# Kernel tuning notes

Measured on AMD Instinct MI355X. Metric: run time of the kernel, lower is better.

## Reference

```python
import jax, jax.numpy as jnp
import numpy as np

EPS = 1e-5
N_GROUPS = 32
N_HEAD = 1


def group_norm(x, gamma, beta):
    B, C, H, W = x.shape
    xg = x.reshape(B, N_GROUPS, C // N_GROUPS, H, W)
    mean = xg.mean(axis=(2, 3, 4), keepdims=True)
    var = xg.var(axis=(2, 3, 4), keepdims=True)
    xg = (xg - mean) * jax.lax.rsqrt(var + EPS)
    x = xg.reshape(B, C, H, W)
    return x * gamma[None, :, None, None] + beta[None, :, None, None]


def setup_inputs() -> dict:
    key = jax.random.key(0)
    k1, k2, k3 = jax.random.split(key, 3)
    B, C, H, W = 32, 512, 32, 32
    x = jax.random.normal(k1, (B, C, H, W), dtype=jnp.float32)
    gamma = jnp.ones((C,), dtype=jnp.float32)
    beta = jnp.zeros((C,), dtype=jnp.float32)
    # fan_avg uniform init for 1x1 convs (bound = sqrt(3*scale/fan_avg))
    bound_qkv = np.sqrt(3.0 / ((C + 3 * C) / 2))
    w_qkv = jax.random.uniform(k2, (3 * C, C), dtype=jnp.float32,
                               minval=-bound_qkv, maxval=bound_qkv)
    b_qkv = jnp.zeros((3 * C,), dtype=jnp.float32)
    bound_out = np.sqrt(3.0 * 1e-10 / C)
    w_out = jax.random.uniform(k3, (C, C), dtype=jnp.float32,
                               minval=-bound_out, maxval=bound_out)
    b_out = jnp.zeros((C,), dtype=jnp.float32)
    return {"x": x, "gamma": gamma, "beta": beta,
            "w_qkv": w_qkv, "b_qkv": b_qkv, "w_out": w_out, "b_out": b_out}


def reference(x, gamma, beta, w_qkv, b_qkv, w_out, b_out):
    B, C, H, W = x.shape
    n_head = N_HEAD
    head_dim = C // n_head
    norm = group_norm(x, gamma, beta)
    # 1x1 conv == channel matmul: [B,3C,H,W]
    qkv = jnp.einsum('bchw,oc->bohw', norm, w_qkv) + b_qkv[None, :, None, None]
    qkv = qkv.reshape(B, n_head, 3 * head_dim, H, W)
    q, k, v = jnp.split(qkv, 3, axis=2)  # each [B,n,hd,H,W]
    scale = 1.0 / np.sqrt(head_dim)
    attn = jnp.einsum('bnchw,bncyx->bnhwyx', q, k) * scale
    attn = jax.nn.softmax(attn.reshape(B, n_head, H, W, H * W), axis=-1)
    attn = attn.reshape(B, n_head, H, W, H, W)
    out = jnp.einsum('bnhwyx,bncyx->bnchw', attn, v).reshape(B, C, H, W)
    out = jnp.einsum('bchw,oc->bohw', out, w_out) + b_out[None, :, None, None]
    return out + x
```

## Files before the change

kernel.cpp:

```cpp
#include <hip/hip_runtime.h>
#include <hip/hip_bf16.h>

#define B_    32
#define C_    512
#define S_    1024
#define G_    32
#define CPG_  16
#define EPS_  1e-5f
#define SCALE_ 0.044194173824159216f

typedef __attribute__((ext_vector_type(4))) float  floatx4;
typedef __attribute__((ext_vector_type(8))) __bf16 bf16x8;

__device__ __forceinline__ float bf2f(unsigned short u) {
    union { unsigned int i; float f; } v; v.i = ((unsigned int)u) << 16; return v.f;
}
__device__ __forceinline__ unsigned short f2bf(float f) {
    union { float f; unsigned int i; } v; v.f = f;
    unsigned int r = v.i + 0x7fffu + ((v.i >> 16) & 1u);
    return (unsigned short)(r >> 16);
}

__device__ __forceinline__ void gl16(const unsigned short* g, unsigned short* l) {
    __builtin_amdgcn_global_load_lds(
        (const __attribute__((address_space(1))) unsigned int*)g,
        (__attribute__((address_space(3))) unsigned int*)l, 16, 0, 0);
}

__global__ __launch_bounds__(256) void gnxnt(const float* __restrict__ x,
                                             const float* __restrict__ gamma,
                                             const float* __restrict__ beta,
                                             unsigned short* __restrict__ xnt,
                                             float* __restrict__ lbuf) {
    const int bid = blockIdx.x;
    const int b = bid >> 5, g = bid & 31;
    if (threadIdx.x < 8)
        ((float4*)lbuf)[bid * 8 + threadIdx.x] = make_float4(0.f, 0.f, 0.f, 0.f);

    __shared__ float tile[16 * 1025];
    __shared__ float a1[4], a2[4];
    const float* xb = x + (size_t)b * (C_ * S_) + (size_t)g * (CPG_ * S_);
    const int t = threadIdx.x;

    float s = 0.f, ss = 0.f;
    #pragma unroll
    for (int k = 0; k < 16; k++) {
        int idx = t + k * 256;
        float4 v = ((const float4*)xb)[idx];
        int c = idx >> 8, s4 = (idx & 255) * 4;
        float* dst = tile + c * 1025 + s4;
        dst[0] = v.x; dst[1] = v.y; dst[2] = v.z; dst[3] = v.w;
        s  += v.x + v.y + v.z + v.w;
        ss += v.x * v.x + v.y * v.y + v.z * v.z + v.w * v.w;
    }
    #pragma unroll
    for (int o = 32; o; o >>= 1) { s += __shfl_down(s, o); ss += __shfl_down(ss, o); }
    const int wid = t >> 6, lane = t & 63;
    if (lane == 0) { a1[wid] = s; a2[wid] = ss; }
    __syncthreads();
    float S  = a1[0] + a1[1] + a1[2] + a1[3];
    float SS = a2[0] + a2[1] + a2[2] + a2[3];
    float mean = S * (1.f / 16384.f);
    float var  = SS * (1.f / 16384.f) - mean * mean;
    float rstd = rsqrtf(var + EPS_);

    const int c0 = g * 16, cc = (t & 3) * 4;
    float av[4], bv[4];
    #pragma unroll
    for (int i = 0; i < 4; i++) {
        float a_ = rstd * gamma[c0 + cc + i];
        av[i] = a_; bv[i] = beta[c0 + cc + i] - mean * a_;
    }
    unsigned short* xo = xnt + (size_t)b * (S_ * C_) + c0 + cc;
    #pragma unroll
    for (int p = 0; p < 16; p++) {
        int srow = p * 64 + (t >> 2);
        const float* col = tile + srow;
        ushort4 o4;
        o4.x = f2bf(av[0] * col[(cc + 0) * 1025] + bv[0]);
        o4.y = f2bf(av[1] * col[(cc + 1) * 1025] + bv[1]);
        o4.z = f2bf(av[2] * col[(cc + 2) * 1025] + bv[2]);
        o4.w = f2bf(av[3] * col[(cc + 3) * 1025] + bv[3]);
        *(ushort4*)(xo + (size_t)srow * C_) = o4;
    }
}

__global__ __launch_bounds__(256) void tcast(const float* __restrict__ w,
                                             const float* __restrict__ w_out,
                                             unsigned short* __restrict__ WqT,
                                             unsigned short* __restrict__ WkT,
                                             unsigned short* __restrict__ WvT,
                                             unsigned short* __restrict__ Woutb) {
    const int z = blockIdx.z;
    const int m0 = blockIdx.y * 64, c0 = blockIdx.x * 64;
    const int t = threadIdx.x, tr = t >> 4, tc4 = (t & 15) * 4;
    if (z == 3) {
        #pragma unroll
        for (int i = 0; i < 4; i++) {
            int r = tr + i * 16;
            float4 v = *(const float4*)(w_out + (size_t)(m0 + r) * 512 + c0 + tc4);
            ushort4 o4;
            o4.x = f2bf(v.x); o4.y = f2bf(v.y); o4.z = f2bf(v.z); o4.w = f2bf(v.w);
            *(ushort4*)(Woutb + (size_t)(m0 + r) * 512 + c0 + tc4) = o4;
        }
        return;
    }
    const float* src = w + (size_t)z * 262144;
    unsigned short* dst = (z == 0) ? WqT : (z == 1) ? WkT : WvT;
    __shared__ float tile[64][65];
    #pragma unroll
    for (int i = 0; i < 4; i++) {
        int r = tr + i * 16;
        float4 v = *(const float4*)(src + (size_t)(m0 + r) * 512 + c0 + tc4);
        tile[r][tc4 + 0] = v.x; tile[r][tc4 + 1] = v.y;
        tile[r][tc4 + 2] = v.z; tile[r][tc4 + 3] = v.w;
    }
    __syncthreads();
    #pragma unroll
    for (int i = 0; i < 4; i++) {
        int sr = tr + i * 16;
        ushort4 o4;
        o4.x = f2bf(tile[tc4 + 0][sr]); o4.y = f2bf(tile[tc4 + 1][sr]);
        o4.z = f2bf(tile[tc4 + 2][sr]); o4.w = f2bf(tile[tc4 + 3][sr]);
        *(ushort4*)(dst + (size_t)(c0 + sr) * 512 + m0 + tc4) = o4;
    }
}

__global__ __launch_bounds__(256) void vecprep(const unsigned short* __restrict__ WkT,
                                               const float* __restrict__ w_out,
                                               const float* __restrict__ b_qkv,
                                               float* __restrict__ bzv) {
    const int o = blockIdx.x, t = threadIdx.x;
    float us = 0.f, bv = 0.f;
    #pragma unroll
    for (int mm = 0; mm < 2; mm++) {
        int m = t + mm * 256;
        us += b_qkv[m] * bf2f(WkT[(size_t)o * 512 + m]);
        bv += w_out[(size_t)o * 512 + m] * b_qkv[1024 + m];
    }
    #pragma unroll
    for (int sh = 32; sh; sh >>= 1) { us += __shfl_down(us, sh); bv += __shfl_down(bv, sh); }
    __shared__ float a[2][4];
    const int wid = t >> 6, lane = t & 63;
    if (lane == 0) { a[0][wid] = us; a[1][wid] = bv; }
    __syncthreads();
    if (t == 0) {
        bzv[o]       = (a[0][0] + a[0][1] + a[0][2] + a[0][3]) * SCALE_;
        bzv[512 + o] =  a[1][0] + a[1][1] + a[1][2] + a[1][3];
    }
}

template<bool SWAP>
__device__ __forceinline__ void mfma_loop(const unsigned short* __restrict__ Ag, int lda,
                                          const unsigned short* __restrict__ Bg, int ldb,
                                          int K, int m0, int n0,
                                          unsigned short* ldsA, unsigned short* ldsB,
                                          floatx4 (&acc)[4][4]) {
    const int t = threadIdx.x, lane = t & 63, wave = t >> 6;
    const int wr = (wave >> 1) * 64, wc = (wave & 1) * 64;
    const int lrow = lane & 15, lq = lane >> 4;
    const int srow = wave * 16 + (lane >> 2);
    const int scol = (lane & 3) * 8;
    const unsigned short* gA0 = Ag + (size_t)(m0 + srow) * lda + scol;
    const unsigned short* gA1 = gA0 + (size_t)64 * lda;
    const unsigned short* gB0 = Bg + (size_t)(n0 + srow) * ldb + scol;
    const unsigned short* gB1 = gB0 + (size_t)64 * ldb;
    unsigned short* lA = ldsA + wave * 512;
    unsigned short* lB = ldsB + wave * 512;
    for (int k0 = 0; k0 < K; k0 += 64) {
        gl16(gA0 + k0,      lA);
        gl16(gA1 + k0,      lA + 2048);
        gl16(gA0 + k0 + 32, lA + 4096);
        gl16(gA1 + k0 + 32, lA + 6144);
        gl16(gB0 + k0,      lB);
        gl16(gB1 + k0,      lB + 2048);
        gl16(gB0 + k0 + 32, lB + 4096);
        gl16(gB1 + k0 + 32, lB + 6144);
        __syncthreads();
        #pragma unroll
        for (int sub = 0; sub < 2; sub++) {
            bf16x8 af[4], bfr[4];
            #pragma unroll
            for (int i = 0; i < 4; i++) {
                af[i]  = *(const bf16x8*)(ldsA + sub * 4096 + (wr + i * 16 + lrow) * 32 + lq * 8);
                bfr[i] = *(const bf16x8*)(ldsB + sub * 4096 + (wc + i * 16 + lrow) * 32 + lq * 8);
            }
            #pragma unroll
            for (int i = 0; i < 4; i++)
                #pragma unroll
                for (int j = 0; j < 4; j++) {
                    if (SWAP)
                        acc[i][j] = __builtin_amdgcn_mfma_f32_16x16x32_bf16(bfr[j], af[i], acc[i][j], 0, 0, 0);
                    else
                        acc[i][j] = __builtin_amdgcn_mfma_f32_16x16x32_bf16(af[i], bfr[j], acc[i][j], 0, 0, 0);
                }
        }
        __syncthreads();
    }
}

__global__ __launch_bounds__(256) void prep_gemm(const unsigned short* __restrict__ WkT,
                                                 const unsigned short* __restrict__ WqT,
                                                 const unsigned short* __restrict__ Woutb,
                                                 const unsigned short* __restrict__ WvT,
                                                 unsigned short* __restrict__ Wzv) {
    __shared__ __align__(16) unsigned short ldsA[2 * 128 * 32];
    __shared__ __align__(16) unsigned short ldsB[2 * 128 * 32];
    const int z = blockIdx.z;
    const int m0 = blockIdx.y * 128, n0 = blockIdx.x * 128;
    const int t = threadIdx.x, lane = t & 63, wave = t >> 6;
    const int wr = (wave >> 1) * 64, wc = (wave & 1) * 64;
    const int lrow = lane & 15, lq = lane >> 4;
    floatx4 acc[4][4];
    #pragma unroll
    for (int i = 0; i < 4; i++)
        #pragma unroll
        for (int j = 0; j < 4; j++) acc[i][j] = (floatx4){0.f, 0.f, 0.f, 0.f};
    const unsigned short* Ag = z ? Woutb : WkT;
    const unsigned short* Bg = z ? WvT   : WqT;
    mfma_loop<true>(Ag, 512, Bg, 512, 512, m0, n0, ldsA, ldsB, acc);
    const float sc = z ? 1.f : SCALE_;
    #pragma unroll
    for (int i = 0; i < 4; i++)
        #pragma unroll
        for (int j = 0; j < 4; j++) {
            int row = z * 512 + m0 + wr + i * 16 + lrow;
            int col = n0 + wc + j * 16 + lq * 4;
            floatx4 v = acc[i][j];
            ushort4 o4;
            o4.x = f2bf(v[0] * sc); o4.y = f2bf(v[1] * sc);
            o4.z = f2bf(v[2] * sc); o4.w = f2bf(v[3] * sc);
            *(ushort4*)(Wzv + (size_t)row * 512 + col) = o4;
        }
}

template<bool SWAP>
__device__ __forceinline__ void mfma256_loop(const unsigned short* __restrict__ Ag, int lda,
                                             const unsigned short* __restrict__ Bg, int ldb,
                                             int nt, int m0, int n0,
                                             unsigned short* lds, floatx4 (&acc)[8][4]) {
    const int tid  = threadIdx.x;
    const int lane = tid & 63, wave = tid >> 6;
    const int wm = wave >> 2, wn = wave & 3;
    const int lrow = lane & 15, lq = lane >> 4;
    const int cs = lq ^ ((lrow >> 1) & 3);

    int aofs[8], bofs[4];
    #pragma unroll
    for (int i = 0; i < 8; i++) aofs[i] = (wm * 128 + i * 16 + lrow) * 32 + cs * 8;
    #pragma unroll
    for (int j = 0; j < 4; j++) bofs[j] = (wn * 64 + j * 16 + lrow) * 32 + cs * 8;

    const int sr  = tid >> 2;
    const int scs = (tid & 3) ^ ((tid >> 3) & 3);
    const unsigned short* gA = Ag + (size_t)(m0 + sr) * lda + scs * 8;
    const unsigned short* gB = Bg + (size_t)(n0 + sr) * ldb + scs * 8;
    const size_t a128 = (size_t)128 * lda, b128 = (size_t)128 * ldb;
    unsigned short* lwA = lds + wave * 512;
    unsigned short* lwB = lds + 32768 + wave * 512;

#define STAGE_A(t, kh) do { \
    unsigned short* lb_ = lwA + ((t) & 1) * 16384 + (kh) * 8192; \
    const unsigned short* gp_ = gA + (t) * 64 + (kh) * 32; \
    gl16(gp_, lb_); gl16(gp_ + a128, lb_ + 4096); } while (0)
#define STAGE_B(t, kh) do { \
    unsigned short* lb_ = lwB + ((t) & 1) * 16384 + (kh) * 8192; \
    const unsigned short* gp_ = gB + (t) * 64 + (kh) * 32; \
    gl16(gp_, lb_); gl16(gp_ + b128, lb_ + 4096); } while (0)

    STAGE_A(0, 0); STAGE_B(0, 0); STAGE_A(0, 1); STAGE_B(0, 1);
    STAGE_A(1, 0); STAGE_B(1, 0);
    asm volatile("s_waitcnt vmcnt(4)" ::: "memory");
    __builtin_amdgcn_s_barrier();

    bf16x8 af[4], bfr[4];
    for (int u = 0; u < nt; ++u) {
        const int p = u & 1;
        #pragma unroll
        for (int ph = 0; ph < 4; ++ph) {
            const int kh = ph >> 1, mh = ph & 1;
            const int slab = p * 16384 + kh * 8192;
            if (mh == 0) {
                #pragma unroll
                for (int j = 0; j < 4; j++)
                    bfr[j] = *(const bf16x8*)(lds + 32768 + slab + bofs[j]);
            }
            #pragma unroll
            for (int i = 0; i < 4; i++)
                af[i] = *(const bf16x8*)(lds + slab + aofs[mh * 4 + i]);
            if (ph == 0)      { if (u + 1 < nt) STAGE_A(u + 1, 1); }
            else if (ph == 1) { if (u + 1 < nt) STAGE_B(u + 1, 1); }
            else if (ph == 2) { if (u + 2 < nt) STAGE_A(u + 2, 0); }
            else              { if (u + 2 < nt) STAGE_B(u + 2, 0); }
            __builtin_amdgcn_s_barrier();
            asm volatile("s_waitcnt lgkmcnt(0)" ::: "memory");
            __builtin_amdgcn_sched_barrier(0);
            __builtin_amdgcn_s_setprio(1);
            #pragma unroll
            for (int i = 0; i < 4; i++)
                #pragma unroll
                for (int j = 0; j < 4; j++) {
                    if (SWAP)
                        acc[mh * 4 + i][j] = __builtin_amdgcn_mfma_f32_16x16x32_bf16(
                            bfr[j], af[i], acc[mh * 4 + i][j], 0, 0, 0);
                    else
                        acc[mh * 4 + i][j] = __builtin_amdgcn_mfma_f32_16x16x32_bf16(
                            af[i], bfr[j], acc[mh * 4 + i][j], 0, 0, 0);
                }
            __builtin_amdgcn_s_setprio(0);
            if (ph < 3) {
                __builtin_amdgcn_s_barrier();
            } else if (u < nt - 2) {
                asm volatile("s_waitcnt vmcnt(4)" ::: "memory");
                __builtin_amdgcn_s_barrier();
            } else if (u == nt - 2) {
                asm volatile("s_waitcnt vmcnt(0)" ::: "memory");
                __builtin_amdgcn_s_barrier();
            }
        }
    }
#undef STAGE_A
#undef STAGE_B
}

#define GEMM256_VARS                                                  \
    __shared__ __align__(16) unsigned short lds[65536];               \
    const int lane = threadIdx.x & 63, wave = threadIdx.x >> 6;       \
    const int wm = wave >> 2, wn = wave & 3;                          \
    const int lrow = lane & 15, lq = lane >> 4;                       \
    floatx4 acc[8][4];                                                \
    _Pragma("unroll") for (int i = 0; i < 8; i++)                     \
        _Pragma("unroll") for (int j = 0; j < 4; j++)                 \
            acc[i][j] = (floatx4){0.f, 0.f, 0.f, 0.f};

__global__ __launch_bounds__(512, 2) void zv_mfma(const unsigned short* __restrict__ Wzv,
                                                  const unsigned short* __restrict__ xnt,
                                                  const float* __restrict__ bzv,
                                                  unsigned short* __restrict__ Zb,
                                                  unsigned short* __restrict__ Vb) {
    const int f = blockIdx.x;
    const int xcd = f & 7, j = f >> 3;
    const int b = xcd + 8 * (j >> 4);
    const int tile = j & 15;
    const int m0 = (tile >> 2) * 256, n0 = (tile & 3) * 256;
    GEMM256_VARS
    const unsigned short* Bg = xnt + (size_t)b * (S_ * C_);
    if (m0 < 512) {
        mfma256_loop<false>(Wzv, C_, Bg, C_, 8, m0, n0, lds, acc);
        unsigned short* dst = Zb + (size_t)b * (S_ * C_);
        #pragma unroll
        for (int i = 0; i < 8; i++)
            #pragma unroll
            for (int j2 = 0; j2 < 4; j2++) {
                int oabs = m0 + wm * 128 + i * 16 + lq * 4;
                int s    = n0 + wn * 64 + j2 * 16 + lrow;
                float4 bi = *(const float4*)(bzv + oabs);
                floatx4 v = acc[i][j2];
                ushort4 o4;
                o4.x = f2bf(v[0] + bi.x); o4.y = f2bf(v[1] + bi.y);
                o4.z = f2bf(v[2] + bi.z); o4.w = f2bf(v[3] + bi.w);
                *(ushort4*)(dst + (size_t)s * C_ + oabs) = o4;
            }
    } else {
        mfma256_loop<true>(Wzv, C_, Bg, C_, 8, m0, n0, lds, acc);
        unsigned short* dst = Vb + (size_t)b * (C_ * S_);
        #pragma unroll
        for (int i = 0; i < 8; i++)
            #pragma unroll
            for (int j2 = 0; j2 < 4; j2++) {
                int row = m0 + wm * 128 + i * 16 + lrow;
                int c   = row - 512;
                int sb  = n0 + wn * 64 + j2 * 16 + lq * 4;
                float bi = bzv[row];
                floatx4 v = acc[i][j2];
                ushort4 o4;
                o4.x = f2bf(v[0] + bi); o4.y = f2bf(v[1] + bi);
                o4.z = f2bf(v[2] + bi); o4.w = f2bf(v[3] + bi);
                *(ushort4*)(dst + (size_t)c * S_ + sb) = o4;
            }
    }
}

__global__ __launch_bounds__(512, 2) void scores_exp(const unsigned short* __restrict__ Zb,
                                                     const unsigned short* __restrict__ xnt,
                                                     unsigned short* __restrict__ Pb,
                                                     float* __restrict__ l) {
    const int f = blockIdx.x;
    const int xcd = f & 7, j = f >> 3;
    const int b = xcd + 8 * (j >> 4);
    const int tile = j & 15;
    const int m0 = (tile >> 2) * 256, n0 = (tile & 3) * 256;
    GEMM256_VARS
    const unsigned short* Ag = Zb  + (size_t)b * (S_ * C_);
    const unsigned short* Bg = xnt + (size_t)b * (S_ * C_);
    mfma256_loop<true>(Ag, C_, Bg, C_, 8, m0, n0, lds, acc);
    unsigned short* pp = Pb + (size_t)b * (S_ * S_);
    float* lb = l + b * S_;
    float rsv[8];
    #pragma unroll
    for (int i = 0; i < 8; i++) {
        int q = m0 + wm * 128 + i * 16 + lrow;
        float rs = 0.f;
        #pragma unroll
        for (int j2 = 0; j2 < 4; j2++) {
            int kv = n0 + wn * 64 + j2 * 16 + lq * 4;
            floatx4 v = acc[i][j2];
            float e0 = __expf(v[0]), e1 = __expf(v[1]);
            float e2 = __expf(v[2]), e3 = __expf(v[3]);
            rs += (e0 + e1) + (e2 + e3);
            ushort4 o4;
            o4.x = f2bf(e0); o4.y = f2bf(e1); o4.z = f2bf(e2); o4.w = f2bf(e3);
            *(ushort4*)(pp + (size_t)q * S_ + kv) = o4;
        }
        rs += __shfl_xor(rs, 16);
        rs += __shfl_xor(rs, 32);
        rsv[i] = rs;
    }
    __syncthreads();
    float* sred = (float*)lds;
    if (lane < 16) {
        #pragma unroll
        for (int i = 0; i < 8; i++)
            sred[wn * 256 + wm * 128 + i * 16 + lrow] = rsv[i];
    }
    __syncthreads();
    if (threadIdx.x < 256) {
        int q = threadIdx.x;
        float sum = (sred[q] + sred[256 + q]) + (sred[512 + q] + sred[768 + q]);
        atomicAdd(lb + m0 + q, sum);
    }
}

__global__ __launch_bounds__(512, 2) void pv_out(const unsigned short* __restrict__ Vb,
                                                 const unsigned short* __restrict__ Pb,
                                                 const float* __restrict__ l,
                                                 const float* __restrict__ bout,
                                                 const float* __restrict__ x,
                                                 float* __restrict__ out) {
    const int f = blockIdx.x;
    const int xcd = f & 7, j = f >> 3;
    const int b = xcd + 8 * (j >> 3);
    const int tile = j & 7;
    const int m0 = (tile & 1) * 256, n0 = (tile >> 1) * 256;
    GEMM256_VARS
    const unsigned short* Ag = Vb + (size_t)b * (C_ * S_);
    const unsigned short* Bg = Pb + (size_t)b * (S_ * S_);
    mfma256_loop<true>(Ag, S_, Bg, S_, 16, m0, n0, lds, acc);
    const float* lb = l + b * S_;
    const float* xb = x + (size_t)b * (C_ * S_);
    float* ob = out + (size_t)b * (C_ * S_);
    #pragma unroll
    for (int i = 0; i < 8; i++) {
        int c = m0 + wm * 128 + i * 16 + lrow;
        float bb = bout[c];
        #pragma unroll
        for (int j2 = 0; j2 < 4; j2++) {
            int s = n0 + wn * 64 + j2 * 16 + lq * 4;
            float4 lv = *(const float4*)(lb + s);
            size_t idx = (size_t)c * S_ + s;
            float4 xv = *(const float4*)(xb + idx);
            floatx4 v = acc[i][j2];
            float4 r;
            r.x = v[0] * __frcp_rn(lv.x) + bb + xv.x;
            r.y = v[1] * __frcp_rn(lv.y) + bb + xv.y;
            r.z = v[2] * __frcp_rn(lv.z) + bb + xv.z;
            r.w = v[3] * __frcp_rn(lv.w) + bb + xv.w;
            *(float4*)(ob + idx) = r;
        }
    }
}

extern "C" void kernel_launch(void* const* d_in, const int* in_sizes, int n_in,
                              void* d_out, int out_size, void* d_ws, size_t ws_size,
                              hipStream_t stream) {
    const float* x      = (const float*)d_in[0];
    const float* gamma  = (const float*)d_in[1];
    const float* beta   = (const float*)d_in[2];
    const float* w_qkv  = (const float*)d_in[3];
    const float* b_qkv  = (const float*)d_in[4];
    const float* w_out  = (const float*)d_in[5];
    const float* b_out  = (const float*)d_in[6];
    float* out          = (float*)d_out;

    char* ws = (char*)d_ws;
    unsigned short* Zb    = (unsigned short*)(ws);
    unsigned short* Vb    = (unsigned short*)(ws + 33554432ULL);
    unsigned short* xnt   = (unsigned short*)(ws + 67108864ULL);
    unsigned short* Pb    = (unsigned short*)(ws + 100663296ULL);
    unsigned short* WqT   = (unsigned short*)(ws + 167772160ULL);
    unsigned short* WkT   = (unsigned short*)(ws + 167772160ULL + 524288ULL);
    unsigned short* WvT   = (unsigned short*)(ws + 167772160ULL + 1048576ULL);
    unsigned short* Woutb = (unsigned short*)(ws + 167772160ULL + 1572864ULL);
    unsigned short* Wzv   = (unsigned short*)(ws + 167772160ULL + 2097152ULL);
    float*          bzv   = (float*)(ws + 167772160ULL + 3145728ULL);
    float*          lbuf  = (float*)(ws + 167772160ULL + 3162112ULL);

    gnxnt    <<<B_ * G_, 256, 0, stream>>>(x, gamma, beta, xnt, lbuf);
    tcast    <<<dim3(8, 8, 4), 256, 0, stream>>>(w_qkv, w_out, WqT, WkT, WvT, Woutb);
    prep_gemm<<<dim3(4, 4, 2), 256, 0, stream>>>(WkT, WqT, Woutb, WvT, Wzv);
    vecprep  <<<512, 256, 0, stream>>>(WkT, w_out, b_qkv, bzv);
    zv_mfma  <<<512, 512, 0, stream>>>(Wzv, xnt, bzv, Zb, Vb);
    scores_exp<<<512, 512, 0, stream>>>(Zb, xnt, Pb, lbuf);
    pv_out   <<<256, 512, 0, stream>>>(Vb, Pb, lbuf, b_out, x, out);
}
```

Baseline: 305.0 us.

## Switch attention GEMM pipeline from bf16 to fp8 with scaling factors

Converts the normalized activations, fused weights, Z/V intermediates and the exponentiated score matrix from bf16 to fp8, and replaces the bf16 MFMA loop with an fp8 16x16x32 MFMA loop using 8-byte operand fragments and a byte-oriented LDS layout. Power-of-two scale factors keep the small-magnitude Z and V values in fp8 range and are undone in the softmax and output epilogues. This halves global and LDS traffic and doubles MFMA throughput per byte. The cost is much lower precision in the score and probability matrices, which may hurt accuracy.

```diff
diff --git a/kernel.cpp b/kernel.cpp
--- a/kernel.cpp
+++ b/kernel.cpp
@@ -8,9 +8,14 @@
 #define CPG_  16
 #define EPS_  1e-5f
 #define SCALE_ 0.044194173824159216f
+#define ZS_    1024.0f
+#define VS_    1048576.0f
+#define INVZS_ 0.0009765625f
+#define INVVS_ 9.5367431640625e-07f
 
 typedef __attribute__((ext_vector_type(4))) float  floatx4;
 typedef __attribute__((ext_vector_type(8))) __bf16 bf16x8;
+typedef long lng;
 
 __device__ __forceinline__ float bf2f(unsigned short u) {
     union { unsigned int i; float f; } v; v.i = ((unsigned int)u) << 16; return v.f;
@@ -20,8 +25,13 @@
     unsigned int r = v.i + 0x7fffu + ((v.i >> 16) & 1u);
     return (unsigned short)(r >> 16);
 }
-
-__device__ __forceinline__ void gl16(const unsigned short* g, unsigned short* l) {
+__device__ __forceinline__ unsigned int f2f8x4(float a, float b, float c, float d) {
+    unsigned int v = (unsigned int)__builtin_amdgcn_cvt_pk_fp8_f32(a, b, 0, false);
+    v = (unsigned int)__builtin_amdgcn_cvt_pk_fp8_f32(c, d, (int)v, true);
+    return v;
+}
+
+__device__ __forceinline__ void gl16(const void* g, void* l) {
     __builtin_amdgcn_global_load_lds(
         (const __attribute__((address_space(1))) unsigned int*)g,
         (__attribute__((address_space(3))) unsigned int*)l, 16, 0, 0);
@@ -30,7 +40,7 @@
 __global__ __launch_bounds__(256) void gnxnt(const float* __restrict__ x,
                                              const float* __restrict__ gamma,
                                              const float* __restrict__ beta,
-                                             unsigned short* __restrict__ xnt,
+                                             unsigned char* __restrict__ xnt,
                                              float* __restrict__ lbuf) {
     const int bid = blockIdx.x;
     const int b = bid >> 5, g = bid & 31;
@@ -71,17 +81,16 @@
         float a_ = rstd * gamma[c0 + cc + i];
         av[i] = a_; bv[i] = beta[c0 + cc + i] - mean * a_;
     }
-    unsigned short* xo = xnt + (size_t)b * (S_ * C_) + c0 + cc;
+    unsigned char* xo = xnt + (size_t)b * (S_ * C_) + c0 + cc;
     #pragma unroll
     for (int p = 0; p < 16; p++) {
         int srow = p * 64 + (t >> 2);
         const float* col = tile + srow;
-        ushort4 o4;
-        o4.x = f2bf(av[0] * col[(cc + 0) * 1025] + bv[0]);
-        o4.y = f2bf(av[1] * col[(cc + 1) * 1025] + bv[1]);
-        o4.z = f2bf(av[2] * col[(cc + 2) * 1025] + bv[2]);
-        o4.w = f2bf(av[3] * col[(cc + 3) * 1025] + bv[3]);
-        *(ushort4*)(xo + (size_t)srow * C_) = o4;
+        unsigned int o4 = f2f8x4(av[0] * col[(cc + 0) * 1025] + bv[0],
+                                 av[1] * col[(cc + 1) * 1025] + bv[1],
+                                 av[2] * col[(cc + 2) * 1025] + bv[2],
+                                 av[3] * col[(cc + 3) * 1025] + bv[3]);
+        *(unsigned int*)(xo + (size_t)srow * C_) = o4;
     }
 }
 
@@ -145,8 +154,8 @@
     if (lane == 0) { a[0][wid] = us; a[1][wid] = bv; }
     __syncthreads();
     if (t == 0) {
-        bzv[o]       = (a[0][0] + a[0][1] + a[0][2] + a[0][3]) * SCALE_;
-        bzv[512 + o] =  a[1][0] + a[1][1] + a[1][2] + a[1][3];
+        bzv[o]       = (a[0][0] + a[0][1] + a[0][2] + a[0][3]) * SCALE_ * ZS_;
+        bzv[512 + o] = (a[1][0] + a[1][1] + a[1][2] + a[1][3]) * VS_;
     }
 }
 
@@ -203,7 +212,7 @@
                                                  const unsigned short* __restrict__ WqT,
                                                  const unsigned short* __restrict__ Woutb,
                                                  const unsigned short* __restrict__ WvT,
-                                                 unsigned short* __restrict__ Wzv) {
+                                                 unsigned char* __restrict__ Wzv) {
     __shared__ __align__(16) unsigned short ldsA[2 * 128 * 32];
     __shared__ __align__(16) unsigned short ldsB[2 * 128 * 32];
     const int z = blockIdx.z;
@@ -219,7 +228,7 @@
     const unsigned short* Ag = z ? Woutb : WkT;
     const unsigned short* Bg = z ? WvT   : WqT;
     mfma_loop<true>(Ag, 512, Bg, 512, 512, m0, n0, ldsA, ldsB, acc);
-    const float sc = z ? 1.f : SCALE_;
+    const float sc = z ? VS_ : (SCALE_ * ZS_);
     #pragma unroll
     for (int i = 0; i < 4; i++)
         #pragma unroll
@@ -227,67 +236,73 @@
             int row = z * 512 + m0 + wr + i * 16 + lrow;
             int col = n0 + wc + j * 16 + lq * 4;
             floatx4 v = acc[i][j];
-            ushort4 o4;
-            o4.x = f2bf(v[0] * sc); o4.y = f2bf(v[1] * sc);
-            o4.z = f2bf(v[2] * sc); o4.w = f2bf(v[3] * sc);
-            *(ushort4*)(Wzv + (size_t)row * 512 + col) = o4;
+            unsigned int o4 = f2f8x4(v[0] * sc, v[1] * sc, v[2] * sc, v[3] * sc);
+            *(unsigned int*)(Wzv + (size_t)row * 512 + col) = o4;
         }
 }
 
 template<bool SWAP>
-__device__ __forceinline__ void mfma256_loop(const unsigned short* __restrict__ Ag, int lda,
-                                             const unsigned short* __restrict__ Bg, int ldb,
-                                             int nt, int m0, int n0,
-                                             unsigned short* lds, floatx4 (&acc)[8][4]) {
+__device__ __forceinline__ void mfma256f8_loop(const unsigned char* __restrict__ Ag, int lda,
+                                               const unsigned char* __restrict__ Bg, int ldb,
+                                               int nt, int m0, int n0,
+                                               unsigned char* lds, floatx4 (&acc)[8][4]) {
     const int tid  = threadIdx.x;
     const int lane = tid & 63, wave = tid >> 6;
     const int wm = wave >> 2, wn = wave & 3;
     const int lrow = lane & 15, lq = lane >> 4;
-    const int cs = lq ^ ((lrow >> 1) & 3);
-
-    int aofs[8], bofs[4];
-    #pragma unroll
-    for (int i = 0; i < 8; i++) aofs[i] = (wm * 128 + i * 16 + lrow) * 32 + cs * 8;
-    #pragma unroll
-    for (int j = 0; j < 4; j++) bofs[j] = (wn * 64 + j * 16 + lrow) * 32 + cs * 8;
+    const int swz  = (lrow >> 1) & 3;
+    const int hb   = (lq & 1) * 8;
+    const int slb  = lq >> 1;
+    const int s0 = ((slb    ) ^ swz) * 16 + hb;
+    const int s1 = ((slb + 2) ^ swz) * 16 + hb;
+
+    int aof[8], bof[4];
+    #pragma unroll
+    for (int i = 0; i < 8; i++) aof[i] = (wm * 128 + i * 16 + lrow) * 64;
+    #pragma unroll
+    for (int j = 0; j < 4; j++) bof[j] = 65536 + (wn * 64 + j * 16 + lrow) * 64;
 
     const int sr  = tid >> 2;
     const int scs = (tid & 3) ^ ((tid >> 3) & 3);
-    const unsigned short* gA = Ag + (size_t)(m0 + sr) * lda + scs * 8;
-    const unsigned short* gB = Bg + (size_t)(n0 + sr) * ldb + scs * 8;
+    const unsigned char* gA = Ag + (size_t)(m0 + sr) * lda + scs * 16;
+    const unsigned char* gB = Bg + (size_t)(n0 + sr) * ldb + scs * 16;
     const size_t a128 = (size_t)128 * lda, b128 = (size_t)128 * ldb;
-    unsigned short* lwA = lds + wave * 512;
-    unsigned short* lwB = lds + 32768 + wave * 512;
+    unsigned char* lwA = lds + wave * 1024;
+    unsigned char* lwB = lds + 65536 + wave * 1024;
 
 #define STAGE_A(t, kh) do { \
-    unsigned short* lb_ = lwA + ((t) & 1) * 16384 + (kh) * 8192; \
-    const unsigned short* gp_ = gA + (t) * 64 + (kh) * 32; \
-    gl16(gp_, lb_); gl16(gp_ + a128, lb_ + 4096); } while (0)
+    unsigned char* lb_ = lwA + ((t) & 1) * 32768 + (kh) * 16384; \
+    const unsigned char* gp_ = gA + (t) * 128 + (kh) * 64; \
+    gl16(gp_, lb_); gl16(gp_ + a128, lb_ + 8192); } while (0)
 #define STAGE_B(t, kh) do { \
-    unsigned short* lb_ = lwB + ((t) & 1) * 16384 + (kh) * 8192; \
-    const unsigned short* gp_ = gB + (t) * 64 + (kh) * 32; \
-    gl16(gp_, lb_); gl16(gp_ + b128, lb_ + 4096); } while (0)
+    unsigned char* lb_ = lwB + ((t) & 1) * 32768 + (kh) * 16384; \
+    const unsigned char* gp_ = gB + (t) * 128 + (kh) * 64; \
+    gl16(gp_, lb_); gl16(gp_ + b128, lb_ + 8192); } while (0)
 
     STAGE_A(0, 0); STAGE_B(0, 0); STAGE_A(0, 1); STAGE_B(0, 1);
     STAGE_A(1, 0); STAGE_B(1, 0);
     asm volatile("s_waitcnt vmcnt(4)" ::: "memory");
     __builtin_amdgcn_s_barrier();
 
-    bf16x8 af[4], bfr[4];
+    lng af0[4], af1[4], bf0[4], bf1[4];
     for (int u = 0; u < nt; ++u) {
         const int p = u & 1;
         #pragma unroll
         for (int ph = 0; ph < 4; ++ph) {
             const int kh = ph >> 1, mh = ph & 1;
-            const int slab = p * 16384 + kh * 8192;
+            const int slab = p * 32768 + kh * 16384;
             if (mh == 0) {
                 #pragma unroll
-                for (int j = 0; j < 4; j++)
-                    bfr[j] = *(const bf16x8*)(lds + 32768 + slab + bofs[j]);
+                for (int j = 0; j < 4; j++) {
+                    bf0[j] = *(const lng*)(lds + slab + bof[j] + s0);
+                    bf1[j] = *(const lng*)(lds + slab + bof[j] + s1);
+                }
             }
             #pragma unroll
-            for (int i = 0; i < 4; i++)
-                af[i] = *(const bf16x8*)(lds + slab + aofs[mh * 4 + i]);
+            for (int i = 0; i < 4; i++) {
+                af0[i] = *(const lng*)(lds + slab + aof[mh * 4 + i] + s0);
+                af1[i] = *(const lng*)(lds + slab + aof[mh * 4 + i] + s1);
+            }
             if (ph == 0)      { if (u + 1 < nt) STAGE_A(u + 1, 1); }
             else if (ph == 1) { if (u + 1 < nt) STAGE_B(u + 1, 1); }
             else if (ph == 2) { if (u + 2 < nt) STAGE_A(u + 2, 0); }
@@ -301,11 +316,22 @@
                 #pragma unroll
                 for (int j = 0; j < 4; j++) {
                     if (SWAP)
-                        acc[mh * 4 + i][j] = __builtin_amdgcn_mfma_f32_16x16x32_bf16(
-                            bfr[j], af[i], acc[mh * 4 + i][j], 0, 0, 0);
+                        acc[mh * 4 + i][j] = __builtin_amdgcn_mfma_f32_16x16x32_fp8_fp8(
+                            bf0[j], af0[i], acc[mh * 4 + i][j], 0, 0, 0);
                     else
-                        acc[mh * 4 + i][j] = __builtin_amdgcn_mfma_f32_16x16x32_bf16(
-                            af[i], bfr[j], acc[mh * 4 + i][j], 0, 0, 0);
+                        acc[mh * 4 + i][j] = __builtin_amdgcn_mfma_f32_16x16x32_fp8_fp8(
+                            af0[i], bf0[j], acc[mh * 4 + i][j], 0, 0, 0);
+                }
+            #pragma unroll
+            for (int i = 0; i < 4; i++)
+                #pragma unroll
+                for (int j = 0; j < 4; j++) {
+                    if (SWAP)
+                        acc[mh * 4 + i][j] = __builtin_amdgcn_mfma_f32_16x16x32_fp8_fp8(
+                            bf1[j], af1[i], acc[mh * 4 + i][j], 0, 0, 0);
+                    else
+                        acc[mh * 4 + i][j] = __builtin_amdgcn_mfma_f32_16x16x32_fp8_fp8(
+                            af1[i], bf1[j], acc[mh * 4 + i][j], 0, 0, 0);
                 }
             __builtin_amdgcn_s_setprio(0);
             if (ph < 3) {
@@ -323,8 +349,8 @@
 #undef STAGE_B
 }
 
-#define GEMM256_VARS                                                  \
-    __shared__ __align__(16) unsigned short lds[65536];               \
+#define GEMMF8_VARS                                                   \
+    __shared__ __align__(16) unsigned char lds[131072];               \
     const int lane = threadIdx.x & 63, wave = threadIdx.x >> 6;       \
     const int wm = wave >> 2, wn = wave & 3;                          \
     const int lrow = lane & 15, lq = lane >> 4;                       \
@@ -333,21 +359,21 @@
         _Pragma("unroll") for (int j = 0; j < 4; j++)                 \
             acc[i][j] = (floatx4){0.f, 0.f, 0.f, 0.f};
 
-__global__ __launch_bounds__(512, 2) void zv_mfma(const unsigned short* __restrict__ Wzv,
-                                                  const unsigned short* __restrict__ xnt,
+__global__ __launch_bounds__(512, 2) void zv_mfma(const unsigned char* __restrict__ Wzv,
+                                                  const unsigned char* __restrict__ xnt,
                                                   const float* __restrict__ bzv,
-                                                  unsigned short* __restrict__ Zb,
-                                                  unsigned short* __restrict__ Vb) {
+                                                  unsigned char* __restrict__ Zb,
+                                                  unsigned char* __restrict__ Vb) {
     const int f = blockIdx.x;
     const int xcd = f & 7, j = f >> 3;
     const int b = xcd + 8 * (j >> 4);
     const int tile = j & 15;
     const int m0 = (tile >> 2) * 256, n0 = (tile & 3) * 256;
-    GEMM256_VARS
-    const unsigned short* Bg = xnt + (size_t)b * (S_ * C_);
+    GEMMF8_VARS
+    const unsigned char* Bg = xnt + (size_t)b * (S_ * C_);
     if (m0 < 512) {
-        mfma256_loop<false>(Wzv, C_, Bg, C_, 8, m0, n0, lds, acc);
-        unsigned short* dst = Zb + (size_t)b * (S_ * C_);
+        mfma256f8_loop<false>(Wzv, C_, Bg, C_, 4, m0, n0, lds, acc);
+        unsigned char* dst = Zb + (size_t)b * (S_ * C_);
         #pragma unroll
         for (int i = 0; i < 8; i++)
             #pragma unroll
@@ -356,14 +382,13 @@
                 int s    = n0 + wn * 64 + j2 * 16 + lrow;
                 float4 bi = *(const float4*)(bzv + oabs);
                 floatx4 v = acc[i][j2];
-                ushort4 o4;
-                o4.x = f2bf(v[0] + bi.x); o4.y = f2bf(v[1] + bi.y);
-                o4.z = f2bf(v[2] + bi.z); o4.w = f2bf(v[3] + bi.w);
-                *(ushort4*)(dst + (size_t)s * C_ + oabs) = o4;
+                unsigned int o4 = f2f8x4(v[0] + bi.x, v[1] + bi.y,
+                                         v[2] + bi.z, v[3] + bi.w);
+                *(unsigned int*)(dst + (size_t)s * C_ + oabs) = o4;
             }
     } else {
-        mfma256_loop<true>(Wzv, C_, Bg, C_, 8, m0, n0, lds, acc);
-        unsigned short* dst = Vb + (size_t)b * (C_ * S_);
+        mfma256f8_loop<true>(Wzv, C_, Bg, C_, 4, m0, n0, lds, acc);
+        unsigned char* dst = Vb + (size_t)b * (C_ * S_);
         #pragma unroll
         for (int i = 0; i < 8; i++)
             #pragma unroll
@@ -373,28 +398,26 @@
                 int sb  = n0 + wn * 64 + j2 * 16 + lq * 4;
                 float bi = bzv[row];
                 floatx4 v = acc[i][j2];
-                ushort4 o4;
-                o4.x = f2bf(v[0] + bi); o4.y = f2bf(v[1] + bi);
-                o4.z = f2bf(v[2] + bi); o4.w = f2bf(v[3] + bi);
-                *(ushort4*)(dst + (size_t)c * S_ + sb) = o4;
+                unsigned int o4 = f2f8x4(v[0] + bi, v[1] + bi, v[2] + bi, v[3] + bi);
+                *(unsigned int*)(dst + (size_t)c * S_ + sb) = o4;
             }
     }
 }
 
-__global__ __launch_bounds__(512, 2) void scores_exp(const unsigned short* __restrict__ Zb,
-                                                     const unsigned short* __restrict__ xnt,
-                                                     unsigned short* __restrict__ Pb,
+__global__ __launch_bounds__(512, 2) void scores_exp(const unsigned char* __restrict__ Zb,
+                                                     const unsigned char* __restrict__ xnt,
+                                                     unsigned char* __restrict__ Pb,
                                                      float* __restrict__ l) {
     const int f = blockIdx.x;
     const int xcd = f & 7, j = f >> 3;
     const int b = xcd + 8 * (j >> 4);
     const int tile = j & 15;
     const int m0 = (tile >> 2) * 256, n0 = (tile & 3) * 256;
-    GEMM256_VARS
-    const unsigned short* Ag = Zb  + (size_t)b * (S_ * C_);
-    const unsigned short* Bg = xnt + (size_t)b * (S_ * C_);
-    mfma256_loop<true>(Ag, C_, Bg, C_, 8, m0, n0, lds, acc);
-    unsigned short* pp = Pb + (size_t)b * (S_ * S_);
+    GEMMF8_VARS
+    const unsigned char* Ag = Zb  + (size_t)b * (S_ * C_);
+    const unsigned char* Bg = xnt + (size_t)b * (S_ * C_);
+    mfma256f8_loop<true>(Ag, C_, Bg, C_, 4, m0, n0, lds, acc);
+    unsigned char* pp = Pb + (size_t)b * ((size_t)S_ * S_);
     float* lb = l + b * S_;
     float rsv[8];
     #pragma unroll
@@ -405,12 +428,10 @@
         for (int j2 = 0; j2 < 4; j2++) {
             int kv = n0 + wn * 64 + j2 * 16 + lq * 4;
             floatx4 v = acc[i][j2];
-            float e0 = __expf(v[0]), e1 = __expf(v[1]);
-            float e2 = __expf(v[2]), e3 = __expf(v[3]);
+            float e0 = __expf(v[0] * INVZS_), e1 = __expf(v[1] * INVZS_);
+            float e2 = __expf(v[2] * INVZS_), e3 = __expf(v[3] * INVZS_);
             rs += (e0 + e1) + (e2 + e3);
-            ushort4 o4;
-            o4.x = f2bf(e0); o4.y = f2bf(e1); o4.z = f2bf(e2); o4.w = f2bf(e3);
-            *(ushort4*)(pp + (size_t)q * S_ + kv) = o4;
+            *(unsigned int*)(pp + (size_t)q * S_ + kv) = f2f8x4(e0, e1, e2, e3);
         }
         rs += __shfl_xor(rs, 16);
         rs += __shfl_xor(rs, 32);
@@ -431,8 +452,8 @@
     }
 }
 
-__global__ __launch_bounds__(512, 2) void pv_out(const unsigned short* __restrict__ Vb,
-                                                 const unsigned short* __restrict__ Pb,
+__global__ __launch_bounds__(512, 2) void pv_out(const unsigned char* __restrict__ Vb,
+                                                 const unsigned char* __restrict__ Pb,
                                                  const float* __restrict__ l,
                                                  const float* __restrict__ bout,
                                                  const float* __restrict__ x,
@@ -442,10 +463,10 @@
     const int b = xcd + 8 * (j >> 3);
     const int tile = j & 7;
     const int m0 = (tile & 1) * 256, n0 = (tile >> 1) * 256;
-    GEMM256_VARS
-    const unsigned short* Ag = Vb + (size_t)b * (C_ * S_);
-    const unsigned short* Bg = Pb + (size_t)b * (S_ * S_);
-    mfma256_loop<true>(Ag, S_, Bg, S_, 16, m0, n0, lds, acc);
+    GEMMF8_VARS
+    const unsigned char* Ag = Vb + (size_t)b * (C_ * S_);
+    const unsigned char* Bg = Pb + (size_t)b * ((size_t)S_ * S_);
+    mfma256f8_loop<true>(Ag, S_, Bg, S_, 8, m0, n0, lds, acc);
     const float* lb = l + b * S_;
     const float* xb = x + (size_t)b * (C_ * S_);
     float* ob = out + (size_t)b * (C_ * S_);
@@ -461,10 +482,10 @@
             float4 xv = *(const float4*)(xb + idx);
             floatx4 v = acc[i][j2];
             float4 r;
-            r.x = v[0] * __frcp_rn(lv.x) + bb + xv.x;
-            r.y = v[1] * __frcp_rn(lv.y) + bb + xv.y;
-            r.z = v[2] * __frcp_rn(lv.z) + bb + xv.z;
-            r.w = v[3] * __frcp_rn(lv.w) + bb + xv.w;
+            r.x = v[0] * (__frcp_rn(lv.x) * INVVS_) + bb + xv.x;
+            r.y = v[1] * (__frcp_rn(lv.y) * INVVS_) + bb + xv.y;
+            r.z = v[2] * (__frcp_rn(lv.z) * INVVS_) + bb + xv.z;
+            r.w = v[3] * (__frcp_rn(lv.w) * INVVS_) + bb + xv.w;
             *(float4*)(ob + idx) = r;
         }
     }
@@ -483,17 +504,17 @@
     float* out          = (float*)d_out;
 
     char* ws = (char*)d_ws;
-    unsigned short* Zb    = (unsigned short*)(ws);
-    unsigned short* Vb    = (unsigned short*)(ws + 33554432ULL);
-    unsigned short* xnt   = (unsigned short*)(ws + 67108864ULL);
-    unsigned short* Pb    = (unsigned short*)(ws + 100663296ULL);
-    unsigned short* WqT   = (unsigned short*)(ws + 167772160ULL);
-    unsigned short* WkT   = (unsigned short*)(ws + 167772160ULL + 524288ULL);
-    unsigned short* WvT   = (unsigned short*)(ws + 167772160ULL + 1048576ULL);
-    unsigned short* Woutb = (unsigned short*)(ws + 167772160ULL + 1572864ULL);
-    unsigned short* Wzv   = (unsigned short*)(ws + 167772160ULL + 2097152ULL);
-    float*          bzv   = (float*)(ws + 167772160ULL + 3145728ULL);
-    float*          lbuf  = (float*)(ws + 167772160ULL + 3162112ULL);
+    unsigned char* Zb    = (unsigned char*)(ws);
+    unsigned char* Vb    = (unsigned char*)(ws + 16777216ULL);
+    unsigned char* xnt   = (unsigned char*)(ws + 33554432ULL);
+    unsigned char* Pb    = (unsigned char*)(ws + 50331648ULL);
+    unsigned short* WqT   = (unsigned short*)(ws + 100663296ULL);
+    unsigned short* WkT   = (unsigned short*)(ws + 100663296ULL + 524288ULL);
+    unsigned short* WvT   = (unsigned short*)(ws + 100663296ULL + 1048576ULL);
+    unsigned short* Woutb = (unsigned short*)(ws + 100663296ULL + 1572864ULL);
+    unsigned char*  Wzv   = (unsigned char*)(ws + 100663296ULL + 2097152ULL);
+    float*          bzv   = (float*)(ws + 100663296ULL + 2621440ULL);
+    float*          lbuf  = (float*)(ws + 100663296ULL + 2629632ULL);
 
     gnxnt    <<<B_ * G_, 256, 0, stream>>>(x, gamma, beta, xnt, lbuf);
     tcast    <<<dim3(8, 8, 4), 256, 0, stream>>>(w_qkv, w_out, WqT, WkT, WvT, Woutb);
```

Measured after the change: 286.3 us. -6.1%, faster.
